# Optimization experiments

Hardware: AMD Instinct MI355X
Metric: run time of the kernel (lower is better)

## Reference

```python
import jax, jax.numpy as jnp
import numpy as np

NUM_BINS = 15       # calibration_cfg['num_prob_bins']
POOL_W = 3          # calibration_cfg['conf_pool_width']
BIN_WIDTH = 1.0 / NUM_BINS  # get_bins(num_prob_bins, 0.0, 1.0)


def _conv(x, w):
    # x: [N,C,H,W], w: [O,I,kh,kw], SAME padding, stride 1
    return jax.lax.conv_general_dilated(
        x, w, (1, 1), 'SAME', dimension_numbers=('NCHW', 'OIHW', 'NCHW'))


def _neighbor_mean(p):
    # agg_neighbors_preds(discrete=False): mean over POOL_W x POOL_W window,
    # border windows averaged over valid pixels only (count_include_pad=False).
    ones_k = jnp.ones((1, 1, POOL_W, POOL_W), p.dtype)
    s = _conv(p, ones_k)
    cnt = _conv(jnp.ones_like(p), ones_k)
    return s / cnt


def setup_inputs() -> dict:
    key = jax.random.key(0)
    k1, k2, k3, k4, k5 = jax.random.split(key, 5)
    N, C, H, W = 32, 3, 512, 512
    context_images = jax.random.normal(k1, (1, N, C, H, W), jnp.float32)
    context_labels = jax.random.uniform(k2, (1, N, 1, H, W), jnp.float32)
    target_logits = jax.random.normal(k3, (1, 1, H, W), jnp.float32)
    # stand-in base_model params (3x3 conv on image + 3x3 conv on LOO label mean)
    w_img = 0.1 * jax.random.normal(k4, (1, C, 3, 3), jnp.float32)
    w_lab = 0.1 * jax.random.normal(k5, (1, 1, 3, 3), jnp.float32)
    return {"context_images": context_images, "context_labels": context_labels,
            "target_logits": target_logits, "w_img": w_img, "w_lab": w_lab}


def reference(context_images, context_labels, target_logits, w_img, w_lab):
    # context_images: [1,N,C,H,W], context_labels: [1,N,1,H,W], target_logits: [1,1,H,W]
    _, N, C, H, W = context_images.shape
    imgs = context_images[0]   # [N,C,H,W] -- each support image is the held-out target once
    labs = context_labels[0]   # [N,1,H,W]

    # --- leave-one-out support predictions (vectorized over the N-iteration loop) ---
    # stand-in base_model: conv(held-out image) + conv(mean of remaining context labels)
    loo_mean = (jnp.sum(labs, axis=0, keepdims=True) - labs) / (N - 1)  # [N,1,H,W]
    support_logits = _conv(imgs, w_img) + _conv(loo_mean, w_lab)        # [N,1,H,W]
    y_probs = jax.nn.sigmoid(support_logits)
    if POOL_W > 1:
        y_probs = _neighbor_mean(y_probs)
    y_true = (labs > 0.5).astype(jnp.float32)                            # [N,1,H,W]

    # --- histogram bin accumulation (update_prob_pixel_meters + prob_bin_stats) ---
    bin_idx = jnp.clip((y_probs / BIN_WIDTH).astype(jnp.int32), 0, NUM_BINS - 1)
    flat_idx = bin_idx.reshape(-1)
    counts = jax.ops.segment_sum(jnp.ones(flat_idx.shape, jnp.float32), flat_idx,
                                 num_segments=NUM_BINS)
    pos = jax.ops.segment_sum(y_true.reshape(-1), flat_idx, num_segments=NUM_BINS)
    bin_freqs = jnp.where(counts > 0, pos / jnp.maximum(counts, 1.0), 0.0)  # [NUM_BINS]

    # --- bin ownership of target probs + gather (get_bin_per_sample) ---
    uncal_probs = jax.nn.sigmoid(target_logits)                 # [1,1,H,W]
    own = jnp.clip((uncal_probs[:, 0] / BIN_WIDTH).astype(jnp.int32),
                   0, NUM_BINS - 1)[:, None]                    # [1,1,H,W]
    return bin_freqs[own]                                       # [1,1,H,W]
```

## Files before the change

### kernel.cpp

```cpp
#include <hip/hip_runtime.h>
#include <hip/hip_bf16.h>

#define NUM_BINS 15
#define N_CTX 32
#define C_IMG 3
#define HGT 512
#define WID 512
#define HW (HGT * WID)

#define SEG 16
#define NSEG (HGT / SEG)
#define UNITS (N_CTX * NSEG)

__global__ __launch_bounds__(256) void k_sumlab(const float4* __restrict__ labs,
                                                float4* __restrict__ sumLab,
                                                unsigned int* __restrict__ hist) {
    int i = blockIdx.x * 256 + threadIdx.x;
    if (blockIdx.x == 0 && threadIdx.x < 2 * NUM_BINS) hist[threadIdx.x] = 0u;
    float4 s = make_float4(0.f, 0.f, 0.f, 0.f);
    #pragma unroll
    for (int n = 0; n < N_CTX; ++n) {
        float4 v = labs[(size_t)n * (HW / 4) + i];
        s.x += v.x; s.y += v.y; s.z += v.z; s.w += v.w;
    }
    sumLab[i] = s;
}

__global__ __launch_bounds__(256, 1) void k_main(const float* __restrict__ imgs,
                                                 const float* __restrict__ labs,
                                                 const float* __restrict__ sumLab,
                                                 const float* __restrict__ w_img,
                                                 const float* __restrict__ w_lab,
                                                 unsigned int* __restrict__ hist) {
    __shared__ unsigned int sh[2 * NUM_BINS];
    const int tid  = threadIdx.x;
    const int lane = tid & 63;
    const int u    = blockIdx.x * 4 + (tid >> 6);
    const int n    = u >> 5;
    const int seg  = u & (NSEG - 1);
    const int y0   = seg * SEG;
    const int x0   = lane * 8;
    const float inv31 = 1.0f / 31.0f;
    const bool l0  = (lane == 0);
    const bool l63 = (lane == 63);

    if (tid < 2 * NUM_BINS) sh[tid] = 0u;
    __syncthreads();

    float w[4][3][3];
    #pragma unroll
    for (int c = 0; c < 3; ++c)
        #pragma unroll
        for (int i = 0; i < 3; ++i)
            #pragma unroll
            for (int j = 0; j < 3; ++j)
                w[c][i][j] = w_img[c * 9 + i * 3 + j];
    #pragma unroll
    for (int i = 0; i < 3; ++i)
        #pragma unroll
        for (int j = 0; j < 3; ++j)
            w[3][i][j] = w_lab[i * 3 + j];

    const float* pi0 = imgs + (size_t)n * C_IMG * HW + x0;
    const float* pi1 = pi0 + HW;
    const float* pi2 = pi0 + 2 * HW;
    const float* pla = labs + (size_t)n * HW + x0;
    const float* psu = sumLab + x0;

    float hA2[8], hA1[8], hB1[8], hs2[8], hs1[8], la1[8], la2[8];
    #pragma unroll
    for (int c = 0; c < 8; ++c) {
        hA2[c] = hA1[c] = hB1[c] = 0.f;
        hs2[c] = hs1[c] = 0.f;
        la1[c] = la2[c] = 0.f;
    }
    unsigned int accC[4] = {0u, 0u, 0u, 0u};
    unsigned int accP[4] = {0u, 0u, 0u, 0u};

    #pragma unroll 2
    for (int it = 0; it < SEG + 4; ++it) {
        const int r = y0 - 2 + it;
        float4 A0, B0, A1, B1, A2, B2, AL, BL, AS, BS;
        if (r >= 0 && r < HGT) {
            const size_t ro = (size_t)r * WID;
            A0 = *reinterpret_cast<const float4*>(pi0 + ro);
            B0 = *reinterpret_cast<const float4*>(pi0 + ro + 4);
            A1 = *reinterpret_cast<const float4*>(pi1 + ro);
            B1 = *reinterpret_cast<const float4*>(pi1 + ro + 4);
            A2 = *reinterpret_cast<const float4*>(pi2 + ro);
            B2 = *reinterpret_cast<const float4*>(pi2 + ro + 4);
            AL = *reinterpret_cast<const float4*>(pla + ro);
            BL = *reinterpret_cast<const float4*>(pla + ro + 4);
            AS = *reinterpret_cast<const float4*>(psu + ro);
            BS = *reinterpret_cast<const float4*>(psu + ro + 4);
        } else {
            const float4 z4 = make_float4(0.f, 0.f, 0.f, 0.f);
            A0 = B0 = A1 = B1 = A2 = B2 = AL = BL = AS = BS = z4;
        }

        float v[4][10];
        v[0][1] = A0.x; v[0][2] = A0.y; v[0][3] = A0.z; v[0][4] = A0.w;
        v[0][5] = B0.x; v[0][6] = B0.y; v[0][7] = B0.z; v[0][8] = B0.w;
        v[1][1] = A1.x; v[1][2] = A1.y; v[1][3] = A1.z; v[1][4] = A1.w;
        v[1][5] = B1.x; v[1][6] = B1.y; v[1][7] = B1.z; v[1][8] = B1.w;
        v[2][1] = A2.x; v[2][2] = A2.y; v[2][3] = A2.z; v[2][4] = A2.w;
        v[2][5] = B2.x; v[2][6] = B2.y; v[2][7] = B2.z; v[2][8] = B2.w;
        v[3][1] = (AS.x - AL.x) * inv31;
        v[3][2] = (AS.y - AL.y) * inv31;
        v[3][3] = (AS.z - AL.z) * inv31;
        v[3][4] = (AS.w - AL.w) * inv31;
        v[3][5] = (BS.x - BL.x) * inv31;
        v[3][6] = (BS.y - BL.y) * inv31;
        v[3][7] = (BS.z - BL.z) * inv31;
        v[3][8] = (BS.w - BL.w) * inv31;
        #pragma unroll
        for (int p = 0; p < 4; ++p) {
            float lft = __shfl_up(v[p][8], 1);
            float rgt = __shfl_down(v[p][1], 1);
            v[p][0] = l0  ? 0.f : lft;
            v[p][9] = l63 ? 0.f : rgt;
        }

        float h0[8], h1[8], h2[8];
        #pragma unroll
        for (int c = 0; c < 8; ++c) { h0[c] = 0.f; h1[c] = 0.f; h2[c] = 0.f; }
        #pragma unroll
        for (int p = 0; p < 4; ++p)
            #pragma unroll
            for (int c = 0; c < 8; ++c) {
                h0[c] += w[p][0][0] * v[p][c] + w[p][0][1] * v[p][c + 1] + w[p][0][2] * v[p][c + 2];
                h1[c] += w[p][1][0] * v[p][c] + w[p][1][1] * v[p][c + 1] + w[p][1][2] * v[p][c + 2];
                h2[c] += w[p][2][0] * v[p][c] + w[p][2][1] * v[p][c + 1] + w[p][2][2] * v[p][c + 2];
            }

        const int y = r - 1;
        const bool yv = (y >= 0) & (y < HGT);
        float pc_[8];
        #pragma unroll
        for (int c = 0; c < 8; ++c) {
            float z = hA2[c] + hB1[c] + h2[c];
            float pr = 1.0f / (1.0f + __expf(-z));
            pc_[c] = yv ? pr : 0.f;
        }
        #pragma unroll
        for (int c = 0; c < 8; ++c) { hA2[c] = hA1[c]; hA1[c] = h0[c]; hB1[c] = h1[c]; }

        float hsv[8];
        {
            float lft = __shfl_up(pc_[7], 1);
            float rgt = __shfl_down(pc_[0], 1);
            float pl_ = l0  ? 0.f : lft;
            float pr_ = l63 ? 0.f : rgt;
            hsv[0] = pl_ + pc_[0] + pc_[1];
            #pragma unroll
            for (int c = 1; c < 7; ++c) hsv[c] = pc_[c - 1] + pc_[c] + pc_[c + 1];
            hsv[7] = pc_[6] + pc_[7] + pr_;
        }

        if (it >= 4) {
            const int yc = r - 2;
            const bool row3 = (yc != 0) & (yc != HGT - 1);
            const float cbi = row3 ? (15.0f / 9.0f) : 2.5f;
            const float cbe = row3 ? 2.5f : 3.75f;
            const float cb0 = l0  ? cbe : cbi;
            const float cb7 = l63 ? cbe : cbi;
            #pragma unroll
            for (int c = 0; c < 8; ++c) {
                const float psum = hs2[c] + hs1[c] + hsv[c];
                const float cb = (c == 0) ? cb0 : ((c == 7) ? cb7 : cbi);
                int b = (int)(psum * cb);
                b = b > NUM_BINS - 1 ? NUM_BINS - 1 : b;
                const unsigned int inc = 1u << ((b & 3) << 3);
                const int rs = b >> 2;
                const bool pos = la2[c] > 0.5f;
                const unsigned int incp = pos ? inc : 0u;
                #pragma unroll
                for (int k = 0; k < 4; ++k) {
                    const bool m = (rs == k);
                    accC[k] += m ? inc : 0u;
                    accP[k] += m ? incp : 0u;
                }
            }
        }

        #pragma unroll
        for (int c = 0; c < 8; ++c) { hs2[c] = hs1[c]; hs1[c] = hsv[c]; }
        la2[0] = la1[0]; la2[1] = la1[1]; la2[2] = la1[2]; la2[3] = la1[3];
        la2[4] = la1[4]; la2[5] = la1[5]; la2[6] = la1[6]; la2[7] = la1[7];
        la1[0] = AL.x; la1[1] = AL.y; la1[2] = AL.z; la1[3] = AL.w;
        la1[4] = BL.x; la1[5] = BL.y; la1[6] = BL.z; la1[7] = BL.w;
    }

    #pragma unroll
    for (int b = 0; b < NUM_BINS; ++b) {
        unsigned int c = (accC[b >> 2] >> ((b & 3) * 8)) & 0xffu;
        unsigned int p = (accP[b >> 2] >> ((b & 3) * 8)) & 0xffu;
        #pragma unroll
        for (int off = 1; off < 64; off <<= 1) {
            c += __shfl_xor(c, off);
            p += __shfl_xor(p, off);
        }
        if (lane == 0) {
            atomicAdd(&sh[b], c);
            atomicAdd(&sh[NUM_BINS + b], p);
        }
    }
    __syncthreads();
    if (tid < 2 * NUM_BINS) {
        unsigned int v = sh[tid];
        if (v) atomicAdd(&hist[tid], v);
    }
}

__global__ __launch_bounds__(256) void k_out(const float4* __restrict__ tl,
                                             const unsigned int* __restrict__ hist,
                                             float4* __restrict__ out) {
    __shared__ float s_f[NUM_BINS];
    const float BIN_W = (float)(1.0 / 15.0);
    int tid = threadIdx.x;
    if (tid < NUM_BINS) {
        unsigned int c = hist[tid];
        unsigned int p = hist[NUM_BINS + tid];
        s_f[tid] = (c > 0u) ? (float)p / (float)c : 0.0f;
    }
    __syncthreads();
    int i = blockIdx.x * 256 + tid;
    float4 t = tl[i];
    float4 o;
    {
        float pr = 1.0f / (1.0f + expf(-t.x));
        int b = (int)(pr / BIN_W); b = b < 0 ? 0 : (b > NUM_BINS - 1 ? NUM_BINS - 1 : b);
        o.x = s_f[b];
    }
    {
        float pr = 1.0f / (1.0f + expf(-t.y));
        int b = (int)(pr / BIN_W); b = b < 0 ? 0 : (b > NUM_BINS - 1 ? NUM_BINS - 1 : b);
        o.y = s_f[b];
    }
    {
        float pr = 1.0f / (1.0f + expf(-t.z));
        int b = (int)(pr / BIN_W); b = b < 0 ? 0 : (b > NUM_BINS - 1 ? NUM_BINS - 1 : b);
        o.z = s_f[b];
    }
    {
        float pr = 1.0f / (1.0f + expf(-t.w));
        int b = (int)(pr / BIN_W); b = b < 0 ? 0 : (b > NUM_BINS - 1 ? NUM_BINS - 1 : b);
        o.w = s_f[b];
    }
    out[i] = o;
}

extern "C" void kernel_launch(void* const* d_in, const int* in_sizes, int n_in,
                              void* d_out, int out_size, void* d_ws, size_t ws_size,
                              hipStream_t stream) {
    const float* imgs  = (const float*)d_in[0];
    const float* labs  = (const float*)d_in[1];
    const float* tlog  = (const float*)d_in[2];
    const float* w_img = (const float*)d_in[3];
    const float* w_lab = (const float*)d_in[4];
    float* out = (float*)d_out;

    float* sumLab = (float*)d_ws;
    unsigned int* hist = (unsigned int*)((char*)d_ws + (size_t)HW * sizeof(float));

    k_sumlab<<<HW / 4 / 256, 256, 0, stream>>>((const float4*)labs, (float4*)sumLab, hist);

    k_main<<<UNITS / 4, 256, 0, stream>>>(imgs, labs, sumLab, w_img, w_lab, hist);

    k_out<<<HW / 4 / 256, 256, 0, stream>>>((const float4*)tlog, hist, (float4*)out);
}
```

Before: 205.2 us.

## Software-pipeline row loads with clamped prefetch and halve segment height

Each loop iteration now prefetches the next row into registers through a clamped-address load. This replaces the branchy, zero-filled conditional load, and out-of-range rows are masked with a multiplier instead. The segment height drops from 16 to 8 rows, which doubles the number of work units, and launch bounds now ask for 2 blocks per CU to raise occupancy. The cost is more halo rows reloaded per unit (relative overhead rises from 4/16 to 4/8) and higher register pressure from holding the prefetched row.

```diff
diff --git a/kernel.cpp b/kernel.cpp
--- a/kernel.cpp
+++ b/kernel.cpp
@@ -8,7 +8,7 @@
 #define WID 512
 #define HW (HGT * WID)
 
-#define SEG 16
+#define SEG 8
 #define NSEG (HGT / SEG)
 #define UNITS (N_CTX * NSEG)
 
@@ -26,7 +26,24 @@
     sumLab[i] = s;
 }
 
-__global__ __launch_bounds__(256, 1) void k_main(const float* __restrict__ imgs,
+__device__ __forceinline__ void load_row(const float* pi0, const float* pi1,
+                                         const float* pi2, const float* pla,
+                                         const float* psu, int r, float4 R[10]) {
+    const int rc = r < 0 ? 0 : (r > HGT - 1 ? HGT - 1 : r);
+    const size_t ro = (size_t)rc * WID;
+    R[0] = *reinterpret_cast<const float4*>(pi0 + ro);
+    R[1] = *reinterpret_cast<const float4*>(pi0 + ro + 4);
+    R[2] = *reinterpret_cast<const float4*>(pi1 + ro);
+    R[3] = *reinterpret_cast<const float4*>(pi1 + ro + 4);
+    R[4] = *reinterpret_cast<const float4*>(pi2 + ro);
+    R[5] = *reinterpret_cast<const float4*>(pi2 + ro + 4);
+    R[6] = *reinterpret_cast<const float4*>(pla + ro);
+    R[7] = *reinterpret_cast<const float4*>(pla + ro + 4);
+    R[8] = *reinterpret_cast<const float4*>(psu + ro);
+    R[9] = *reinterpret_cast<const float4*>(psu + ro + 4);
+}
+
+__global__ __launch_bounds__(256, 2) void k_main(const float* __restrict__ imgs,
                                                  const float* __restrict__ labs,
                                                  const float* __restrict__ sumLab,
                                                  const float* __restrict__ w_img,
@@ -36,7 +53,7 @@
     const int tid  = threadIdx.x;
     const int lane = tid & 63;
     const int u    = blockIdx.x * 4 + (tid >> 6);
-    const int n    = u >> 5;
+    const int n    = u >> 6;
     const int seg  = u & (NSEG - 1);
     const int y0   = seg * SEG;
     const int x0   = lane * 8;
@@ -77,42 +94,34 @@
     unsigned int accC[4] = {0u, 0u, 0u, 0u};
     unsigned int accP[4] = {0u, 0u, 0u, 0u};
 
+    float4 C[10];
+    load_row(pi0, pi1, pi2, pla, psu, y0 - 2, C);
+
     #pragma unroll 2
     for (int it = 0; it < SEG + 4; ++it) {
         const int r = y0 - 2 + it;
-        float4 A0, B0, A1, B1, A2, B2, AL, BL, AS, BS;
-        if (r >= 0 && r < HGT) {
-            const size_t ro = (size_t)r * WID;
-            A0 = *reinterpret_cast<const float4*>(pi0 + ro);
-            B0 = *reinterpret_cast<const float4*>(pi0 + ro + 4);
-            A1 = *reinterpret_cast<const float4*>(pi1 + ro);
-            B1 = *reinterpret_cast<const float4*>(pi1 + ro + 4);
-            A2 = *reinterpret_cast<const float4*>(pi2 + ro);
-            B2 = *reinterpret_cast<const float4*>(pi2 + ro + 4);
-            AL = *reinterpret_cast<const float4*>(pla + ro);
-            BL = *reinterpret_cast<const float4*>(pla + ro + 4);
-            AS = *reinterpret_cast<const float4*>(psu + ro);
-            BS = *reinterpret_cast<const float4*>(psu + ro + 4);
-        } else {
-            const float4 z4 = make_float4(0.f, 0.f, 0.f, 0.f);
-            A0 = B0 = A1 = B1 = A2 = B2 = AL = BL = AS = BS = z4;
-        }
+
+        float4 P[10];
+        load_row(pi0, pi1, pi2, pla, psu, r + 1, P);
+
+        const float m = (r >= 0 && r < HGT) ? 1.0f : 0.0f;
+        const float inv31m = inv31 * m;
 
         float v[4][10];
-        v[0][1] = A0.x; v[0][2] = A0.y; v[0][3] = A0.z; v[0][4] = A0.w;
-        v[0][5] = B0.x; v[0][6] = B0.y; v[0][7] = B0.z; v[0][8] = B0.w;
-        v[1][1] = A1.x; v[1][2] = A1.y; v[1][3] = A1.z; v[1][4] = A1.w;
-        v[1][5] = B1.x; v[1][6] = B1.y; v[1][7] = B1.z; v[1][8] = B1.w;
-        v[2][1] = A2.x; v[2][2] = A2.y; v[2][3] = A2.z; v[2][4] = A2.w;
-        v[2][5] = B2.x; v[2][6] = B2.y; v[2][7] = B2.z; v[2][8] = B2.w;
-        v[3][1] = (AS.x - AL.x) * inv31;
-        v[3][2] = (AS.y - AL.y) * inv31;
-        v[3][3] = (AS.z - AL.z) * inv31;
-        v[3][4] = (AS.w - AL.w) * inv31;
-        v[3][5] = (BS.x - BL.x) * inv31;
-        v[3][6] = (BS.y - BL.y) * inv31;
-        v[3][7] = (BS.z - BL.z) * inv31;
-        v[3][8] = (BS.w - BL.w) * inv31;
+        v[0][1] = C[0].x * m; v[0][2] = C[0].y * m; v[0][3] = C[0].z * m; v[0][4] = C[0].w * m;
+        v[0][5] = C[1].x * m; v[0][6] = C[1].y * m; v[0][7] = C[1].z * m; v[0][8] = C[1].w * m;
+        v[1][1] = C[2].x * m; v[1][2] = C[2].y * m; v[1][3] = C[2].z * m; v[1][4] = C[2].w * m;
+        v[1][5] = C[3].x * m; v[1][6] = C[3].y * m; v[1][7] = C[3].z * m; v[1][8] = C[3].w * m;
+        v[2][1] = C[4].x * m; v[2][2] = C[4].y * m; v[2][3] = C[4].z * m; v[2][4] = C[4].w * m;
+        v[2][5] = C[5].x * m; v[2][6] = C[5].y * m; v[2][7] = C[5].z * m; v[2][8] = C[5].w * m;
+        v[3][1] = (C[8].x - C[6].x) * inv31m;
+        v[3][2] = (C[8].y - C[6].y) * inv31m;
+        v[3][3] = (C[8].z - C[6].z) * inv31m;
+        v[3][4] = (C[8].w - C[6].w) * inv31m;
+        v[3][5] = (C[9].x - C[7].x) * inv31m;
+        v[3][6] = (C[9].y - C[7].y) * inv31m;
+        v[3][7] = (C[9].z - C[7].z) * inv31m;
+        v[3][8] = (C[9].w - C[7].w) * inv31m;
         #pragma unroll
         for (int p = 0; p < 4; ++p) {
             float lft = __shfl_up(v[p][8], 1);
@@ -176,19 +185,20 @@
                 const unsigned int incp = pos ? inc : 0u;
                 #pragma unroll
                 for (int k = 0; k < 4; ++k) {
-                    const bool m = (rs == k);
-                    accC[k] += m ? inc : 0u;
-                    accP[k] += m ? incp : 0u;
+                    const bool mm = (rs == k);
+                    accC[k] += mm ? inc : 0u;
+                    accP[k] += mm ? incp : 0u;
                 }
             }
         }
 
         #pragma unroll
-        for (int c = 0; c < 8; ++c) { hs2[c] = hs1[c]; hs1[c] = hsv[c]; }
-        la2[0] = la1[0]; la2[1] = la1[1]; la2[2] = la1[2]; la2[3] = la1[3];
-        la2[4] = la1[4]; la2[5] = la1[5]; la2[6] = la1[6]; la2[7] = la1[7];
-        la1[0] = AL.x; la1[1] = AL.y; la1[2] = AL.z; la1[3] = AL.w;
-        la1[4] = BL.x; la1[5] = BL.y; la1[6] = BL.z; la1[7] = BL.w;
+        for (int c = 0; c < 8; ++c) { hs2[c] = hs1[c]; hs1[c] = hsv[c]; la2[c] = la1[c]; }
+        la1[0] = C[6].x * m; la1[1] = C[6].y * m; la1[2] = C[6].z * m; la1[3] = C[6].w * m;
+        la1[4] = C[7].x * m; la1[5] = C[7].y * m; la1[6] = C[7].z * m; la1[7] = C[7].w * m;
+
+        #pragma unroll
+        for (int q = 0; q < 10; ++q) C[q] = P[q];
     }
 
     #pragma unroll
@@ -207,8 +217,8 @@
     }
     __syncthreads();
     if (tid < 2 * NUM_BINS) {
-        unsigned int v = sh[tid];
-        if (v) atomicAdd(&hist[tid], v);
+        unsigned int vsum = sh[tid];
+        if (vsum) atomicAdd(&hist[tid], vsum);
     }
 }
 
```

Result: no change. 202.7 us (-1.2%).

## Shrink row segments, prefetch next row, specialize edge units, raise occupancy

Applied to the files above, without the earlier changes.

Each wave now handles 4 rows instead of 16, with launch bounds raised to allow four blocks per CU. Each iteration issues the loads for the next row before doing the current row's math. Interior segments take a template path with no boundary branches or bin-scale selection, and labels are packed into a bitmask instead of carried as floats. The sigmoid uses a hardware reciprocal. The smaller segments trade more halo-row reloads (8 of 4 rows recomputed overlap) for better parallelism and latency hiding.

```diff
diff --git a/kernel.cpp b/kernel.cpp
--- a/kernel.cpp
+++ b/kernel.cpp
@@ -1,5 +1,4 @@
 #include <hip/hip_runtime.h>
-#include <hip/hip_bf16.h>
 
 #define NUM_BINS 15
 #define N_CTX 32
@@ -8,7 +7,7 @@
 #define WID 512
 #define HW (HGT * WID)
 
-#define SEG 16
+#define SEG 4
 #define NSEG (HGT / SEG)
 #define UNITS (N_CTX * NSEG)
 
@@ -26,93 +25,73 @@
     sumLab[i] = s;
 }
 
-__global__ __launch_bounds__(256, 1) void k_main(const float* __restrict__ imgs,
-                                                 const float* __restrict__ labs,
-                                                 const float* __restrict__ sumLab,
-                                                 const float* __restrict__ w_img,
-                                                 const float* __restrict__ w_lab,
-                                                 unsigned int* __restrict__ hist) {
-    __shared__ unsigned int sh[2 * NUM_BINS];
-    const int tid  = threadIdx.x;
-    const int lane = tid & 63;
-    const int u    = blockIdx.x * 4 + (tid >> 6);
-    const int n    = u >> 5;
-    const int seg  = u & (NSEG - 1);
-    const int y0   = seg * SEG;
-    const int x0   = lane * 8;
-    const float inv31 = 1.0f / 31.0f;
+template<bool EDGE>
+__device__ __forceinline__ void unit_body(const float* __restrict__ pi0,
+                                          const float* __restrict__ pi1,
+                                          const float* __restrict__ pi2,
+                                          const float* __restrict__ pla,
+                                          const float* __restrict__ psu,
+                                          int y0, int lane,
+                                          const float (&w)[4][3][3],
+                                          unsigned int (&accC)[4],
+                                          unsigned int (&accP)[4]) {
     const bool l0  = (lane == 0);
     const bool l63 = (lane == 63);
-
-    if (tid < 2 * NUM_BINS) sh[tid] = 0u;
-    __syncthreads();
-
-    float w[4][3][3];
-    #pragma unroll
-    for (int c = 0; c < 3; ++c)
-        #pragma unroll
-        for (int i = 0; i < 3; ++i)
-            #pragma unroll
-            for (int j = 0; j < 3; ++j)
-                w[c][i][j] = w_img[c * 9 + i * 3 + j];
-    #pragma unroll
-    for (int i = 0; i < 3; ++i)
-        #pragma unroll
-        for (int j = 0; j < 3; ++j)
-            w[3][i][j] = w_lab[i * 3 + j];
-
-    const float* pi0 = imgs + (size_t)n * C_IMG * HW + x0;
-    const float* pi1 = pi0 + HW;
-    const float* pi2 = pi0 + 2 * HW;
-    const float* pla = labs + (size_t)n * HW + x0;
-    const float* psu = sumLab + x0;
-
-    float hA2[8], hA1[8], hB1[8], hs2[8], hs1[8], la1[8], la2[8];
-    #pragma unroll
-    for (int c = 0; c < 8; ++c) {
-        hA2[c] = hA1[c] = hB1[c] = 0.f;
-        hs2[c] = hs1[c] = 0.f;
-        la1[c] = la2[c] = 0.f;
-    }
-    unsigned int accC[4] = {0u, 0u, 0u, 0u};
-    unsigned int accP[4] = {0u, 0u, 0u, 0u};
+    const float inv31 = 1.0f / 31.0f;
+
+    float hA2[8], hA1[8], hB1[8], hs2[8], hs1[8];
+    #pragma unroll
+    for (int c = 0; c < 8; ++c) { hA2[c] = hA1[c] = hB1[c] = 0.f; hs2[c] = hs1[c] = 0.f; }
+    unsigned int pm1 = 0u, pm2 = 0u;
+
+    float4 C[10];
+    auto loadC = [&](int rr) {
+        int rc = rr;
+        if (EDGE) rc = rr < 0 ? 0 : (rr > HGT - 1 ? HGT - 1 : rr);
+        const size_t ro = (size_t)rc * WID;
+        C[0] = *reinterpret_cast<const float4*>(pi0 + ro);
+        C[1] = *reinterpret_cast<const float4*>(pi0 + ro + 4);
+        C[2] = *reinterpret_cast<const float4*>(pi1 + ro);
+        C[3] = *reinterpret_cast<const float4*>(pi1 + ro + 4);
+        C[4] = *reinterpret_cast<const float4*>(pi2 + ro);
+        C[5] = *reinterpret_cast<const float4*>(pi2 + ro + 4);
+        C[6] = *reinterpret_cast<const float4*>(pla + ro);
+        C[7] = *reinterpret_cast<const float4*>(pla + ro + 4);
+        C[8] = *reinterpret_cast<const float4*>(psu + ro);
+        C[9] = *reinterpret_cast<const float4*>(psu + ro + 4);
+    };
+
+    loadC(y0 - 2);
+    float mcur = 1.f;
+    if (EDGE) mcur = (y0 - 2 >= 0 && y0 - 2 < HGT) ? 1.f : 0.f;
 
     #pragma unroll 2
     for (int it = 0; it < SEG + 4; ++it) {
         const int r = y0 - 2 + it;
-        float4 A0, B0, A1, B1, A2, B2, AL, BL, AS, BS;
-        if (r >= 0 && r < HGT) {
-            const size_t ro = (size_t)r * WID;
-            A0 = *reinterpret_cast<const float4*>(pi0 + ro);
-            B0 = *reinterpret_cast<const float4*>(pi0 + ro + 4);
-            A1 = *reinterpret_cast<const float4*>(pi1 + ro);
-            B1 = *reinterpret_cast<const float4*>(pi1 + ro + 4);
-            A2 = *reinterpret_cast<const float4*>(pi2 + ro);
-            B2 = *reinterpret_cast<const float4*>(pi2 + ro + 4);
-            AL = *reinterpret_cast<const float4*>(pla + ro);
-            BL = *reinterpret_cast<const float4*>(pla + ro + 4);
-            AS = *reinterpret_cast<const float4*>(psu + ro);
-            BS = *reinterpret_cast<const float4*>(psu + ro + 4);
-        } else {
-            const float4 z4 = make_float4(0.f, 0.f, 0.f, 0.f);
-            A0 = B0 = A1 = B1 = A2 = B2 = AL = BL = AS = BS = z4;
-        }
+        const float mm  = EDGE ? mcur : 1.0f;
+        const float i31 = EDGE ? inv31 * mcur : inv31;
+
+        unsigned int pm0 = (C[6].x > 0.5f ? 1u : 0u)  | (C[6].y > 0.5f ? 2u : 0u)
+                         | (C[6].z > 0.5f ? 4u : 0u)  | (C[6].w > 0.5f ? 8u : 0u)
+                         | (C[7].x > 0.5f ? 16u : 0u) | (C[7].y > 0.5f ? 32u : 0u)
+                         | (C[7].z > 0.5f ? 64u : 0u) | (C[7].w > 0.5f ? 128u : 0u);
+        if (EDGE) pm0 = (mcur == 0.f) ? 0u : pm0;
 
         float v[4][10];
-        v[0][1] = A0.x; v[0][2] = A0.y; v[0][3] = A0.z; v[0][4] = A0.w;
-        v[0][5] = B0.x; v[0][6] = B0.y; v[0][7] = B0.z; v[0][8] = B0.w;
-        v[1][1] = A1.x; v[1][2] = A1.y; v[1][3] = A1.z; v[1][4] = A1.w;
-        v[1][5] = B1.x; v[1][6] = B1.y; v[1][7] = B1.z; v[1][8] = B1.w;
-        v[2][1] = A2.x; v[2][2] = A2.y; v[2][3] = A2.z; v[2][4] = A2.w;
-        v[2][5] = B2.x; v[2][6] = B2.y; v[2][7] = B2.z; v[2][8] = B2.w;
-        v[3][1] = (AS.x - AL.x) * inv31;
-        v[3][2] = (AS.y - AL.y) * inv31;
-        v[3][3] = (AS.z - AL.z) * inv31;
-        v[3][4] = (AS.w - AL.w) * inv31;
-        v[3][5] = (BS.x - BL.x) * inv31;
-        v[3][6] = (BS.y - BL.y) * inv31;
-        v[3][7] = (BS.z - BL.z) * inv31;
-        v[3][8] = (BS.w - BL.w) * inv31;
+        v[0][1] = C[0].x * mm; v[0][2] = C[0].y * mm; v[0][3] = C[0].z * mm; v[0][4] = C[0].w * mm;
+        v[0][5] = C[1].x * mm; v[0][6] = C[1].y * mm; v[0][7] = C[1].z * mm; v[0][8] = C[1].w * mm;
+        v[1][1] = C[2].x * mm; v[1][2] = C[2].y * mm; v[1][3] = C[2].z * mm; v[1][4] = C[2].w * mm;
+        v[1][5] = C[3].x * mm; v[1][6] = C[3].y * mm; v[1][7] = C[3].z * mm; v[1][8] = C[3].w * mm;
+        v[2][1] = C[4].x * mm; v[2][2] = C[4].y * mm; v[2][3] = C[4].z * mm; v[2][4] = C[4].w * mm;
+        v[2][5] = C[5].x * mm; v[2][6] = C[5].y * mm; v[2][7] = C[5].z * mm; v[2][8] = C[5].w * mm;
+        v[3][1] = (C[8].x - C[6].x) * i31;
+        v[3][2] = (C[8].y - C[6].y) * i31;
+        v[3][3] = (C[8].z - C[6].z) * i31;
+        v[3][4] = (C[8].w - C[6].w) * i31;
+        v[3][5] = (C[9].x - C[7].x) * i31;
+        v[3][6] = (C[9].y - C[7].y) * i31;
+        v[3][7] = (C[9].z - C[7].z) * i31;
+        v[3][8] = (C[9].w - C[7].w) * i31;
         #pragma unroll
         for (int p = 0; p < 4; ++p) {
             float lft = __shfl_up(v[p][8], 1);
@@ -133,13 +112,15 @@
                 h2[c] += w[p][2][0] * v[p][c] + w[p][2][1] * v[p][c + 1] + w[p][2][2] * v[p][c + 2];
             }
 
-        const int y = r - 1;
-        const bool yv = (y >= 0) & (y < HGT);
+        if (it < SEG + 3) loadC(r + 1);
+        if (EDGE) mcur = (r + 1 >= 0 && r + 1 < HGT) ? 1.f : 0.f;
+
+        const bool yv = EDGE ? (r - 1 >= 0 && r - 1 < HGT) : true;
         float pc_[8];
         #pragma unroll
         for (int c = 0; c < 8; ++c) {
             float z = hA2[c] + hB1[c] + h2[c];
-            float pr = 1.0f / (1.0f + __expf(-z));
+            float pr = __builtin_amdgcn_rcpf(1.0f + __expf(-z));
             pc_[c] = yv ? pr : 0.f;
         }
         #pragma unroll
@@ -158,12 +139,19 @@
         }
 
         if (it >= 4) {
-            const int yc = r - 2;
-            const bool row3 = (yc != 0) & (yc != HGT - 1);
-            const float cbi = row3 ? (15.0f / 9.0f) : 2.5f;
-            const float cbe = row3 ? 2.5f : 3.75f;
+            float cbi, cbe;
+            if (EDGE) {
+                const int yc = r - 2;
+                const bool row3 = (yc != 0) & (yc != HGT - 1);
+                cbi = row3 ? (15.0f / 9.0f) : 2.5f;
+                cbe = row3 ? 2.5f : 3.75f;
+            } else {
+                cbi = 15.0f / 9.0f;
+                cbe = 2.5f;
+            }
             const float cb0 = l0  ? cbe : cbi;
             const float cb7 = l63 ? cbe : cbi;
+            const unsigned int posm = pm2;
             #pragma unroll
             for (int c = 0; c < 8; ++c) {
                 const float psum = hs2[c] + hs1[c] + hsv[c];
@@ -172,24 +160,67 @@
                 b = b > NUM_BINS - 1 ? NUM_BINS - 1 : b;
                 const unsigned int inc = 1u << ((b & 3) << 3);
                 const int rs = b >> 2;
-                const bool pos = la2[c] > 0.5f;
-                const unsigned int incp = pos ? inc : 0u;
+                const unsigned int incp = ((posm >> c) & 1u) ? inc : 0u;
                 #pragma unroll
                 for (int k = 0; k < 4; ++k) {
-                    const bool m = (rs == k);
-                    accC[k] += m ? inc : 0u;
-                    accP[k] += m ? incp : 0u;
+                    const bool mk = (rs == k);
+                    accC[k] += mk ? inc : 0u;
+                    accP[k] += mk ? incp : 0u;
                 }
             }
         }
 
         #pragma unroll
         for (int c = 0; c < 8; ++c) { hs2[c] = hs1[c]; hs1[c] = hsv[c]; }
-        la2[0] = la1[0]; la2[1] = la1[1]; la2[2] = la1[2]; la2[3] = la1[3];
-        la2[4] = la1[4]; la2[5] = la1[5]; la2[6] = la1[6]; la2[7] = la1[7];
-        la1[0] = AL.x; la1[1] = AL.y; la1[2] = AL.z; la1[3] = AL.w;
-        la1[4] = BL.x; la1[5] = BL.y; la1[6] = BL.z; la1[7] = BL.w;
-    }
+        pm2 = pm1; pm1 = pm0;
+    }
+}
+
+__global__ __launch_bounds__(256, 4) void k_main(const float* __restrict__ imgs,
+                                                 const float* __restrict__ labs,
+                                                 const float* __restrict__ sumLab,
+                                                 const float* __restrict__ w_img,
+                                                 const float* __restrict__ w_lab,
+                                                 unsigned int* __restrict__ hist) {
+    __shared__ unsigned int sh[2 * NUM_BINS];
+    const int tid  = threadIdx.x;
+    const int lane = tid & 63;
+    const int u    = blockIdx.x * 4 + (tid >> 6);
+    const int n    = u >> 7;
+    const int seg  = u & (NSEG - 1);
+    const int y0   = seg * SEG;
+    const int x0   = lane * 8;
+
+    if (tid < 2 * NUM_BINS) sh[tid] = 0u;
+    __syncthreads();
+
+    float w[4][3][3];
+    #pragma unroll
+    for (int c = 0; c < 3; ++c)
+        #pragma unroll
+        for (int i = 0; i < 3; ++i)
+            #pragma unroll
+            for (int j = 0; j < 3; ++j)
+                w[c][i][j] = w_img[c * 9 + i * 3 + j];
+    #pragma unroll
+    for (int i = 0; i < 3; ++i)
+        #pragma unroll
+        for (int j = 0; j < 3; ++j)
+            w[3][i][j] = w_lab[i * 3 + j];
+
+    const float* pi0 = imgs + (size_t)n * C_IMG * HW + x0;
+    const float* pi1 = pi0 + HW;
+    const float* pi2 = pi0 + 2 * HW;
+    const float* pla = labs + (size_t)n * HW + x0;
+    const float* psu = sumLab + x0;
+
+    unsigned int accC[4] = {0u, 0u, 0u, 0u};
+    unsigned int accP[4] = {0u, 0u, 0u, 0u};
+
+    if (seg == 0 || seg == NSEG - 1)
+        unit_body<true>(pi0, pi1, pi2, pla, psu, y0, lane, w, accC, accP);
+    else
+        unit_body<false>(pi0, pi1, pi2, pla, psu, y0, lane, w, accC, accP);
 
     #pragma unroll
     for (int b = 0; b < NUM_BINS; ++b) {
@@ -207,8 +238,8 @@
     }
     __syncthreads();
     if (tid < 2 * NUM_BINS) {
-        unsigned int v = sh[tid];
-        if (v) atomicAdd(&hist[tid], v);
+        unsigned int vsum = sh[tid];
+        if (vsum) atomicAdd(&hist[tid], vsum);
     }
 }
 
```

Result: slower. 612.8 us (+198.7%).
